# Optimization experiments

Hardware: AMD Instinct MI355X
Metric: run time of the kernel (lower is better)

## Reference

```python
import jax, jax.numpy as jnp
import numpy as np

LN_EPS = 1e-5

def _layernorm(x, scale, bias):
    mu = jnp.mean(x, axis=-1, keepdims=True)
    var = jnp.var(x, axis=-1, keepdims=True)
    return (x - mu) * jax.lax.rsqrt(var + LN_EPS) * scale + bias

def setup_inputs() -> dict:
    T, node_num, num_nodes, E, C = 4, 10000, 50000, 256, 128
    key = jax.random.key(0)
    ks = jax.random.split(key, 12)
    s = lambda fan_in: 1.0 / np.sqrt(fan_in)
    return {
        "x": jax.random.normal(ks[0], (T * node_num, E), jnp.float32),
        "batched_x": jax.random.normal(ks[1], (num_nodes, E), jnp.float32),
        "indices": jax.random.randint(ks[2], (T, node_num), 0, num_nodes, jnp.int32),
        "ln_d_scale": jnp.ones((E,), jnp.float32),
        "ln_d_bias": jnp.zeros((E,), jnp.float32),
        "W1_d": jax.random.normal(ks[3], (E, 2 * E), jnp.float32) * s(E),
        "b1_d": jnp.zeros((2 * E,), jnp.float32),
        "W2_d": jax.random.normal(ks[4], (2 * E, C), jnp.float32) * s(2 * E),
        "b2_d": jnp.zeros((C,), jnp.float32),
        "ln_u_scale": jnp.ones((C,), jnp.float32),
        "ln_u_bias": jnp.zeros((C,), jnp.float32),
        "W1_u": jax.random.normal(ks[5], (C, 2 * C), jnp.float32) * s(C),
        "b1_u": jnp.zeros((2 * C,), jnp.float32),
        "W2_u": jax.random.normal(ks[6], (2 * C, E), jnp.float32) * s(2 * C),
        "b2_u": jnp.zeros((E,), jnp.float32),
    }

def reference(x, batched_x, indices, ln_d_scale, ln_d_bias, W1_d, b1_d, W2_d, b2_d,
              ln_u_scale, ln_u_bias, W1_u, b1_u, W2_u, b2_u):
    T, node_num = indices.shape
    num_nodes, E = batched_x.shape
    xr = x.reshape(T, node_num, E)
    # _to_entire: per-step scatter-add of active-node embeddings into the full node table
    def scatter_one(xi, idx):
        return jnp.zeros((num_nodes, E), x.dtype).at[idx].add(xi)
    ta = jax.vmap(scatter_one)(xr, indices)          # [T, num_nodes, E]
    inp = ta + batched_x[None]                        # broadcast entire features
    h = _layernorm(inp, ln_d_scale, ln_d_bias)
    h = jax.nn.gelu(h @ W1_d + b1_d, approximate=False) @ W2_d + b2_d  # [T, num_nodes, C]
    # _from_entire: gather each step's active nodes back, concat, LN + MLP up
    g = jnp.take_along_axis(h, indices[..., None], axis=1)  # [T, node_num, C]
    g = g.reshape(T * node_num, -1)
    g = _layernorm(g, ln_u_scale, ln_u_bias)
    out = jax.nn.gelu(g @ W1_u + b1_u, approximate=False) @ W2_u + b2_u  # [T*node_num, E]
    return out
```

## Files before the change

### kernel.cpp

```cpp
#include <hip/hip_runtime.h>
#include <math.h>

#define T_STEPS   4
#define NODE_NUM  10000
#define NUM_NODES 50000
#define E         256
#define TWO_E     512
#define CC        128
#define TWO_C     256
#define ROWS      32

typedef short bf16x8 __attribute__((ext_vector_type(8)));
typedef float f32x4  __attribute__((ext_vector_type(4)));

#define MFMA16(a, b, c) __builtin_amdgcn_mfma_f32_16x16x32_bf16((a), (b), (c), 0, 0, 0)

static __device__ unsigned short g_wt[294912];
static __device__ int g_cnt[T_STEPS * NUM_NODES];

__device__ __forceinline__ float geluf(float v) {
    return 0.5f * v * (1.0f + erff(v * 0.70710678118654752440f));
}

__device__ __forceinline__ unsigned short f2bf(float f) {
    unsigned int u = __builtin_bit_cast(unsigned int, f);
    u += 0x7fffu + ((u >> 16) & 1u);
    return (unsigned short)(u >> 16);
}

__global__ void prep_weights(const float* __restrict__ W1d, const float* __restrict__ W2d,
                             const float* __restrict__ W1u, const float* __restrict__ W2u) {
    int i = blockIdx.x * 256 + threadIdx.x;
    if (i < T_STEPS * NUM_NODES) g_cnt[i] = 0;
    if (i < 131072) {
        int n = i >> 8, k = i & 255;
        g_wt[i] = f2bf(W1d[(size_t)k * TWO_E + n]);
    }
    if (i < 65536) {
        int n = i >> 9, k = i & 511;
        g_wt[131072 + i] = f2bf(W2d[(size_t)k * CC + n]);
    }
    if (i < 32768) {
        int n = i >> 7, k = i & 127;
        g_wt[196608 + i] = f2bf(W1u[(size_t)k * TWO_C + n]);
    }
    if (i < 65536) {
        int n = i >> 8, k = i & 255;
        g_wt[229376 + i] = f2bf(W2u[(size_t)k * E + n]);
    }
}

__global__ void count_kernel(const int* __restrict__ indices) {
    int gr = blockIdx.x * 256 + threadIdx.x;
    if (gr < T_STEPS * NODE_NUM) {
        int t = gr / NODE_NUM;
        atomicAdd(&g_cnt[t * NUM_NODES + indices[gr]], 1);
    }
}

__global__ void zero_dup_kernel(float* __restrict__ table,
                                const int* __restrict__ indices,
                                int gr0, int t0) {
    int gr = gr0 + blockIdx.x * 4 + (threadIdx.x >> 6);
    int t = gr / NODE_NUM;
    int idx = indices[gr];
    if (g_cnt[t * NUM_NODES + idx] < 2) return;
    int c = (threadIdx.x & 63) * 4;
    float4 z = make_float4(0.f, 0.f, 0.f, 0.f);
    *reinterpret_cast<float4*>(&table[((size_t)(t - t0) * NUM_NODES + idx) * E + c]) = z;
}

__global__ void scatter_dup_kernel(float* __restrict__ table,
                                   const float* __restrict__ x,
                                   const int* __restrict__ indices,
                                   int gr0, int t0) {
    int gr = gr0 + blockIdx.x;
    int t = gr / NODE_NUM;
    int idx = indices[gr];
    if (g_cnt[t * NUM_NODES + idx] < 2) return;
    atomicAdd(&table[((size_t)(t - t0) * NUM_NODES + idx) * E + threadIdx.x],
              x[(size_t)gr * E + threadIdx.x]);
}

__global__ __launch_bounds__(256, 3)
void mlp_kernel(const float* __restrict__ table,
                const float* __restrict__ x,
                const float* __restrict__ batched_x,
                const int* __restrict__ indices,
                const float* __restrict__ lnd_s, const float* __restrict__ lnd_b,
                const float* __restrict__ b1d, const float* __restrict__ b2d,
                const float* __restrict__ lnu_s, const float* __restrict__ lnu_b,
                const float* __restrict__ b1u, const float* __restrict__ b2u,
                float* __restrict__ out,
                int gr0, int t0, int grLim) {
    __shared__ __align__(16) unsigned char smem[50176];
    __shared__ const float* rptr[ROWS];
    __shared__ int    ridx[ROWS];

    float*          Xf  = (float*)smem;
    unsigned short* Xs  = (unsigned short*)(smem + 33280);
    unsigned short* H1  = (unsigned short*)smem;
    float*          H2f = (float*)(smem + 33280);
    unsigned short* H2b = (unsigned short*)smem;
    unsigned short* G1  = (unsigned short*)(smem + 8704);

    const unsigned short* w1t  = g_wt;
    const unsigned short* w2t  = g_wt + 131072;
    const unsigned short* w1ut = g_wt + 196608;
    const unsigned short* w2ut = g_wt + 229376;

    const int tid = threadIdx.x;
    const int w = tid >> 6, lane = tid & 63;
    const int l16 = lane & 15, quad = lane >> 4;
    const int grb = gr0 + blockIdx.x * ROWS;

    if (tid < ROWS) {
        int gr = grb + tid;
        if (gr >= grLim) gr = grLim - 1;
        int t = gr / NODE_NUM;
        int idx = indices[gr];
        ridx[tid] = idx;
        rptr[tid] = (g_cnt[t * NUM_NODES + idx] > 1)
            ? (table + ((size_t)(t - t0) * NUM_NODES + idx) * E)
            : (x + (size_t)gr * E);
    }
    __syncthreads();

    #pragma unroll
    for (int it = 0; it < 8; ++it) {
        int v = it * 256 + tid;
        int r = v >> 6;
        int c = (v & 63) * 4;
        float4 tv = *reinterpret_cast<const float4*>(rptr[r] + c);
        float4 bv = *reinterpret_cast<const float4*>(&batched_x[(size_t)ridx[r] * E + c]);
        float4 s; s.x = tv.x + bv.x; s.y = tv.y + bv.y; s.z = tv.z + bv.z; s.w = tv.w + bv.w;
        *reinterpret_cast<float4*>(&Xf[r * 260 + c]) = s;
    }
    __syncthreads();

    {
        int row = tid >> 3, l8 = tid & 7;
        float s = 0.f, sq = 0.f;
        #pragma unroll
        for (int k = 0; k < 32; ++k) {
            float v = Xf[row * 260 + k * 8 + l8];
            s += v; sq += v * v;
        }
        s  += __shfl_xor(s, 1);  s  += __shfl_xor(s, 2);  s  += __shfl_xor(s, 4);
        sq += __shfl_xor(sq, 1); sq += __shfl_xor(sq, 2); sq += __shfl_xor(sq, 4);
        float mu = s * (1.0f / E);
        float var = sq * (1.0f / E) - mu * mu;
        float rs = rsqrtf(var + 1e-5f);
        #pragma unroll
        for (int k = 0; k < 32; ++k) {
            int c = k * 8 + l8;
            float v = (Xf[row * 260 + c] - mu) * rs * lnd_s[c] + lnd_b[c];
            Xs[row * 264 + c] = f2bf(v);
        }
    }
    __syncthreads();

    {
        bf16x8 af[2][8];
        #pragma unroll
        for (int mt = 0; mt < 2; ++mt) {
            const unsigned short* base = Xs + (l16 + 16 * mt) * 264 + quad * 8;
            #pragma unroll
            for (int ks = 0; ks < 8; ++ks)
                af[mt][ks] = *reinterpret_cast<const bf16x8*>(base + ks * 32);
        }
        #pragma unroll
        for (int nt_ = 0; nt_ < 8; ++nt_) {
            int n = (w * 8 + nt_) * 16 + l16;
            const unsigned short* bp = w1t + (size_t)n * 256 + quad * 8;
            f32x4 a0 = {0.f, 0.f, 0.f, 0.f}, a1 = {0.f, 0.f, 0.f, 0.f};
            #pragma unroll
            for (int ks = 0; ks < 8; ++ks) {
                bf16x8 b = *reinterpret_cast<const bf16x8*>(bp + ks * 32);
                a0 = MFMA16(af[0][ks], b, a0);
                a1 = MFMA16(af[1][ks], b, a1);
            }
            float bias = b1d[n];
            #pragma unroll
            for (int reg = 0; reg < 4; ++reg) {
                int r = quad * 4 + reg;
                H1[r * 520 + n]        = f2bf(geluf(a0[reg] + bias));
                H1[(r + 16) * 520 + n] = f2bf(geluf(a1[reg] + bias));
            }
        }
    }
    __syncthreads();

    {
        f32x4 acc2[2][2];
        #pragma unroll
        for (int i = 0; i < 2; ++i)
            #pragma unroll
            for (int j = 0; j < 2; ++j) acc2[i][j] = (f32x4){0.f, 0.f, 0.f, 0.f};
        #pragma unroll
        for (int kh = 0; kh < 2; ++kh) {
            bf16x8 af2[2][8];
            #pragma unroll
            for (int mt = 0; mt < 2; ++mt) {
                const unsigned short* base = H1 + (l16 + 16 * mt) * 520 + kh * 256 + quad * 8;
                #pragma unroll
                for (int ks = 0; ks < 8; ++ks)
                    af2[mt][ks] = *reinterpret_cast<const bf16x8*>(base + ks * 32);
            }
            #pragma unroll
            for (int nt2 = 0; nt2 < 2; ++nt2) {
                int n = (w * 2 + nt2) * 16 + l16;
                const unsigned short* bp = w2t + (size_t)n * 512 + kh * 256 + quad * 8;
                #pragma unroll
                for (int ks = 0; ks < 8; ++ks) {
                    bf16x8 b = *reinterpret_cast<const bf16x8*>(bp + ks * 32);
                    acc2[nt2][0] = MFMA16(af2[0][ks], b, acc2[nt2][0]);
                    acc2[nt2][1] = MFMA16(af2[1][ks], b, acc2[nt2][1]);
                }
            }
        }
        #pragma unroll
        for (int nt2 = 0; nt2 < 2; ++nt2) {
            int n = (w * 2 + nt2) * 16 + l16;
            float bias = b2d[n];
            #pragma unroll
            for (int mt = 0; mt < 2; ++mt)
                #pragma unroll
                for (int reg = 0; reg < 4; ++reg) {
                    int r = mt * 16 + quad * 4 + reg;
                    H2f[r * 132 + n] = acc2[nt2][mt][reg] + bias;
                }
        }
    }
    __syncthreads();

    {
        int row = tid >> 3, l8 = tid & 7;
        float s = 0.f, sq = 0.f;
        #pragma unroll
        for (int k = 0; k < 16; ++k) {
            float v = H2f[row * 132 + k * 8 + l8];
            s += v; sq += v * v;
        }
        s  += __shfl_xor(s, 1);  s  += __shfl_xor(s, 2);  s  += __shfl_xor(s, 4);
        sq += __shfl_xor(sq, 1); sq += __shfl_xor(sq, 2); sq += __shfl_xor(sq, 4);
        float mu = s * (1.0f / CC);
        float var = sq * (1.0f / CC) - mu * mu;
        float rs = rsqrtf(var + 1e-5f);
        #pragma unroll
        for (int k = 0; k < 16; ++k) {
            int c = k * 8 + l8;
            float v = (H2f[row * 132 + c] - mu) * rs * lnu_s[c] + lnu_b[c];
            H2b[row * 136 + c] = f2bf(v);
        }
    }
    __syncthreads();

    {
        bf16x8 af3[2][4];
        #pragma unroll
        for (int mt = 0; mt < 2; ++mt) {
            const unsigned short* base = H2b + (l16 + 16 * mt) * 136 + quad * 8;
            #pragma unroll
            for (int ks = 0; ks < 4; ++ks)
                af3[mt][ks] = *reinterpret_cast<const bf16x8*>(base + ks * 32);
        }
        #pragma unroll
        for (int nt_ = 0; nt_ < 4; ++nt_) {
            int n = (w * 4 + nt_) * 16 + l16;
            const unsigned short* bp = w1ut + (size_t)n * 128 + quad * 8;
            f32x4 a0 = {0.f, 0.f, 0.f, 0.f}, a1 = {0.f, 0.f, 0.f, 0.f};
            #pragma unroll
            for (int ks = 0; ks < 4; ++ks) {
                bf16x8 b = *reinterpret_cast<const bf16x8*>(bp + ks * 32);
                a0 = MFMA16(af3[0][ks], b, a0);
                a1 = MFMA16(af3[1][ks], b, a1);
            }
            float bias = b1u[n];
            #pragma unroll
            for (int reg = 0; reg < 4; ++reg) {
                int r = quad * 4 + reg;
                G1[r * 264 + n]        = f2bf(geluf(a0[reg] + bias));
                G1[(r + 16) * 264 + n] = f2bf(geluf(a1[reg] + bias));
            }
        }
    }
    __syncthreads();

    {
        bf16x8 af4[2][8];
        #pragma unroll
        for (int mt = 0; mt < 2; ++mt) {
            const unsigned short* base = G1 + (l16 + 16 * mt) * 264 + quad * 8;
            #pragma unroll
            for (int ks = 0; ks < 8; ++ks)
                af4[mt][ks] = *reinterpret_cast<const bf16x8*>(base + ks * 32);
        }
        #pragma unroll
        for (int nt_ = 0; nt_ < 4; ++nt_) {
            int n = (w * 4 + nt_) * 16 + l16;
            const unsigned short* bp = w2ut + (size_t)n * 256 + quad * 8;
            f32x4 a0 = {0.f, 0.f, 0.f, 0.f}, a1 = {0.f, 0.f, 0.f, 0.f};
            #pragma unroll
            for (int ks = 0; ks < 8; ++ks) {
                bf16x8 b = *reinterpret_cast<const bf16x8*>(bp + ks * 32);
                a0 = MFMA16(af4[0][ks], b, a0);
                a1 = MFMA16(af4[1][ks], b, a1);
            }
            float bias = b2u[n];
            #pragma unroll
            for (int reg = 0; reg < 4; ++reg) {
                int r = quad * 4 + reg;
                int g0 = grb + r, g1 = grb + r + 16;
                if (g0 < grLim) out[(size_t)g0 * E + n] = a0[reg] + bias;
                if (g1 < grLim) out[(size_t)g1 * E + n] = a1[reg] + bias;
            }
        }
    }
}

extern "C" void kernel_launch(void* const* d_in, const int* in_sizes, int n_in,
                              void* d_out, int out_size, void* d_ws, size_t ws_size,
                              hipStream_t stream) {
    const float* x     = (const float*)d_in[0];
    const float* bx    = (const float*)d_in[1];
    const int*   idxp  = (const int*)  d_in[2];
    const float* lnd_s = (const float*)d_in[3];
    const float* lnd_b = (const float*)d_in[4];
    const float* W1d   = (const float*)d_in[5];
    const float* b1d   = (const float*)d_in[6];
    const float* W2d   = (const float*)d_in[7];
    const float* b2d   = (const float*)d_in[8];
    const float* lnu_s = (const float*)d_in[9];
    const float* lnu_b = (const float*)d_in[10];
    const float* W1u   = (const float*)d_in[11];
    const float* b1u   = (const float*)d_in[12];
    const float* W2u   = (const float*)d_in[13];
    const float* b2u   = (const float*)d_in[14];
    float* out = (float*)d_out;
    float* table = (float*)d_ws;

    const size_t slice_bytes = (size_t)NUM_NODES * E * sizeof(float);
    int tb = (int)(ws_size / slice_bytes);
    if (tb < 1) tb = 1;
    if (tb > T_STEPS) tb = T_STEPS;

    prep_weights<<<784, 256, 0, stream>>>(W1d, W2d, W1u, W2u);
    count_kernel<<<(T_STEPS * NODE_NUM + 255) / 256, 256, 0, stream>>>(idxp);

    for (int t0 = 0; t0 < T_STEPS; t0 += tb) {
        int tcur = T_STEPS - t0 < tb ? T_STEPS - t0 : tb;
        int nrows = tcur * NODE_NUM;
        int gr0 = t0 * NODE_NUM;
        int grLim = gr0 + nrows;
        zero_dup_kernel   <<<nrows / 4, 256, 0, stream>>>(table, idxp, gr0, t0);
        scatter_dup_kernel<<<nrows, E, 0, stream>>>(table, x, idxp, gr0, t0);
        mlp_kernel<<<(nrows + ROWS - 1) / ROWS, 256, 0, stream>>>(
            table, x, bx, idxp, lnd_s, lnd_b, b1d, b2d,
            lnu_s, lnu_b, b1u, b2u, out, gr0, t0, grLim);
    }
}
```

Before: 293.0 us.

## Compact duplicate rows into a list and use a tanh-style sigmoid GELU

Replaces the zero and scatter kernels, which launched one block per gathered row and exited early for non-duplicates, with a compaction pass. That pass records duplicate rows in a global list via an atomic counter and zeroes their table rows, followed by a fixed-size grid that scatter-adds only the listed rows. This removes most of the empty block launches. Separately, the exact erf-based GELU is replaced with a sigmoid approximation of the tanh GELU using fast exp, which cuts transcendental cost but changes numerics relative to the exact-erf reference.

New measurement: 294.9 us. Within noise of the previous version (+0.6%).

```diff
diff --git a/kernel.cpp b/kernel.cpp
--- a/kernel.cpp
+++ b/kernel.cpp
@@ -17,9 +17,12 @@
 
 static __device__ unsigned short g_wt[294912];
 static __device__ int g_cnt[T_STEPS * NUM_NODES];
+static __device__ int g_dup[T_STEPS * NODE_NUM];
+static __device__ int g_ndup[T_STEPS];
 
 __device__ __forceinline__ float geluf(float v) {
-    return 0.5f * v * (1.0f + erff(v * 0.70710678118654752440f));
+    float p = v * (1.5957691216057308f + 0.07135481282636226f * v * v);
+    return v / (1.0f + __expf(-p));
 }
 
 __device__ __forceinline__ unsigned short f2bf(float f) {
@@ -32,6 +35,7 @@
                              const float* __restrict__ W1u, const float* __restrict__ W2u) {
     int i = blockIdx.x * 256 + threadIdx.x;
     if (i < T_STEPS * NUM_NODES) g_cnt[i] = 0;
+    if (i < T_STEPS) g_ndup[i] = 0;
     if (i < 131072) {
         int n = i >> 8, k = i & 255;
         g_wt[i] = f2bf(W1d[(size_t)k * TWO_E + n]);
@@ -58,28 +62,34 @@
     }
 }
 
-__global__ void zero_dup_kernel(float* __restrict__ table,
-                                const int* __restrict__ indices,
-                                int gr0, int t0) {
-    int gr = gr0 + blockIdx.x * 4 + (threadIdx.x >> 6);
+__global__ void compact_zero_kernel(float* __restrict__ table,
+                                    const int* __restrict__ indices,
+                                    int gr0, int t0, int grLim, int slab) {
+    int gr = gr0 + blockIdx.x * 256 + threadIdx.x;
+    if (gr >= grLim) return;
     int t = gr / NODE_NUM;
     int idx = indices[gr];
     if (g_cnt[t * NUM_NODES + idx] < 2) return;
-    int c = (threadIdx.x & 63) * 4;
+    int pos = atomicAdd(&g_ndup[slab], 1);
+    g_dup[gr0 + pos] = gr;
+    float4* rp = reinterpret_cast<float4*>(&table[((size_t)(t - t0) * NUM_NODES + idx) * E]);
     float4 z = make_float4(0.f, 0.f, 0.f, 0.f);
-    *reinterpret_cast<float4*>(&table[((size_t)(t - t0) * NUM_NODES + idx) * E + c]) = z;
-}
-
-__global__ void scatter_dup_kernel(float* __restrict__ table,
-                                   const float* __restrict__ x,
-                                   const int* __restrict__ indices,
-                                   int gr0, int t0) {
-    int gr = gr0 + blockIdx.x;
-    int t = gr / NODE_NUM;
-    int idx = indices[gr];
-    if (g_cnt[t * NUM_NODES + idx] < 2) return;
-    atomicAdd(&table[((size_t)(t - t0) * NUM_NODES + idx) * E + threadIdx.x],
-              x[(size_t)gr * E + threadIdx.x]);
+    #pragma unroll
+    for (int k = 0; k < 64; ++k) rp[k] = z;
+}
+
+__global__ void scatter_list_kernel(float* __restrict__ table,
+                                    const float* __restrict__ x,
+                                    const int* __restrict__ indices,
+                                    int gr0, int t0, int slab) {
+    int nd = g_ndup[slab];
+    for (int e = blockIdx.x; e < nd; e += gridDim.x) {
+        int gr = g_dup[gr0 + e];
+        int t = gr / NODE_NUM;
+        int idx = indices[gr];
+        atomicAdd(&table[((size_t)(t - t0) * NUM_NODES + idx) * E + threadIdx.x],
+                  x[(size_t)gr * E + threadIdx.x]);
+    }
 }
 
 __global__ __launch_bounds__(256, 3)
@@ -353,8 +363,10 @@
         int nrows = tcur * NODE_NUM;
         int gr0 = t0 * NODE_NUM;
         int grLim = gr0 + nrows;
-        zero_dup_kernel   <<<nrows / 4, 256, 0, stream>>>(table, idxp, gr0, t0);
-        scatter_dup_kernel<<<nrows, E, 0, stream>>>(table, x, idxp, gr0, t0);
+        int slab = t0 / tb;
+        compact_zero_kernel<<<(nrows + 255) / 256, 256, 0, stream>>>(
+            table, idxp, gr0, t0, grLim, slab);
+        scatter_list_kernel<<<1024, E, 0, stream>>>(table, x, idxp, gr0, t0, slab);
         mlp_kernel<<<(nrows + ROWS - 1) / ROWS, 256, 0, stream>>>(
             table, x, bx, idxp, lnd_s, lnd_b, b1d, b2d,
             lnu_s, lnu_b, b1u, b2u, out, gr0, t0, grLim);
```
